# Performance work log

Measured on AMD Instinct MI355X. Metric: run time of the kernel, lower is better.

## Reference

```python
import jax, jax.numpy as jnp
import numpy as np

K = 100
TEMPERATURE = 1.0


def setup_inputs() -> dict:
    key = jax.random.key(0)
    k1, k2, k3 = jax.random.split(key, 3)
    student_emb = jax.random.normal(k1, (8, 512, 1500), dtype=jnp.float32)
    teacher_codes = jax.random.randint(k2, (8, 1500), 0, 4096, dtype=jnp.int64)
    codebook = jax.random.normal(k3, (4096, 512), dtype=jnp.float32)
    return {"student_emb": student_emb, "teacher_codes": teacher_codes, "codebook": codebook}


def reference(student_emb, teacher_codes, codebook):
    B, C, T = student_emb.shape
    # flatten tokens: (N, C) with N = B*T
    emb = jnp.transpose(student_emb, (0, 2, 1)).reshape(-1, C)
    codes = teacher_codes.reshape(-1).astype(jnp.int32)

    # Euclidean cdist via the ||a||^2 + ||b||^2 - 2ab expansion (same math as torch.cdist)
    emb_sq = jnp.sum(emb * emb, axis=1, keepdims=True)            # (N,1)
    cb_sq = jnp.sum(codebook * codebook, axis=1)[None, :]         # (1,V)
    d2 = emb_sq + cb_sq - 2.0 * jnp.matmul(emb, codebook.T)       # (N,V)
    distances = jnp.sqrt(jnp.maximum(d2, 0.0))

    # top-k smallest distances
    _, top_k_indices = jax.lax.top_k(-distances, K)               # (N,K)

    # include_correct: replace last candidate with the true code if absent
    correct_in_topk = jnp.any(top_k_indices == codes[:, None], axis=1)
    top_k_indices = top_k_indices.at[:, -1].set(
        jnp.where(correct_in_topk, top_k_indices[:, -1], codes))

    candidate_distances = jnp.take_along_axis(distances, top_k_indices, axis=1)
    logits = -candidate_distances / TEMPERATURE                   # (N,K)

    match = top_k_indices == codes[:, None]
    local_labels = jnp.argmax(match.astype(jnp.int32), axis=1)    # (N,)

    logp = jax.nn.log_softmax(logits, axis=1)
    loss = -jnp.mean(jnp.take_along_axis(logp, local_labels[:, None], axis=1))

    local_predictions = jnp.argmax(logits, axis=-1)
    local_accuracy = jnp.mean((local_predictions == local_labels).astype(jnp.float32))
    global_predictions = jnp.argmin(distances, axis=-1)
    global_accuracy = jnp.mean((global_predictions == codes).astype(jnp.float32))
    correct_in_candidates = jnp.mean(jnp.any(top_k_indices == codes[:, None], axis=1).astype(jnp.float32))

    return loss, local_accuracy, global_accuracy, correct_in_candidates
```

## Files before the change

### kernel.cpp

```cpp
#include <hip/hip_runtime.h>
#include <hip/hip_bf16.h>
#include <cstdint>

#define B_ 8
#define C_ 512
#define T_ 1500
#define N_ (B_*T_)
#define NPAD_ 12032
#define V_ 4096
#define K_ 100

typedef unsigned long long u64;
typedef __attribute__((ext_vector_type(8))) short short8;
typedef __attribute__((ext_vector_type(8))) unsigned short u16x8;
typedef __attribute__((ext_vector_type(4))) float f32x4;

__device__ __forceinline__ unsigned short f2bf(float x){
    __hip_bfloat16 h = __float2bfloat16(x);
    return __builtin_bit_cast(unsigned short, h);
}
__device__ __forceinline__ unsigned short f2h(float x){
    return __builtin_bit_cast(unsigned short, (_Float16)x);
}
__device__ __forceinline__ float h2f(unsigned short h){
    return (float)__builtin_bit_cast(_Float16, h);
}

__device__ __forceinline__ void gll16(const unsigned short* g, unsigned short* l){
    __builtin_amdgcn_global_load_lds(
        (const __attribute__((address_space(1))) void*)g,
        (__attribute__((address_space(3))) void*)l, 16, 0, 0);
}

__global__ __launch_bounds__(256) void cbconv_kernel(const float* __restrict__ CB,
                                                     unsigned short* __restrict__ CBh,
                                                     float* __restrict__ csq){
    int wv = threadIdx.x >> 6, lane = threadIdx.x & 63;
    int r = blockIdx.x * 4 + wv;
    const float4* p4 = (const float4*)(CB + (size_t)r * C_);
    ushort4* o4 = (ushort4*)(CBh + (size_t)r * C_);
    float s = 0.f;
    #pragma unroll
    for (int j = 0; j < 2; ++j){
        float4 v = p4[lane + j*64];
        s += v.x*v.x + v.y*v.y + v.z*v.z + v.w*v.w;
        ushort4 h; h.x = f2bf(v.x); h.y = f2bf(v.y); h.z = f2bf(v.z); h.w = f2bf(v.w);
        o4[lane + j*64] = h;
    }
    #pragma unroll
    for (int o = 32; o; o >>= 1) s += __shfl_down(s, o, 64);
    if (lane == 0) csq[r] = s;
}

__global__ __launch_bounds__(256) void transpose_conv_kernel(const float* __restrict__ S,
                                                             unsigned short* __restrict__ embT,
                                                             float* __restrict__ esq){
    __shared__ float tile[32][33];
    __shared__ float psum[8][33];
    int b  = blockIdx.z;
    int c0 = blockIdx.y * 32;
    int t0 = blockIdx.x * 32;
    int tx = threadIdx.x, ty = threadIdx.y;
    #pragma unroll
    for (int r = 0; r < 4; ++r){
        int c = c0 + ty + r*8;
        int t = t0 + tx;
        tile[ty + r*8][tx] = (t < T_) ? S[((size_t)b*C_ + c)*T_ + t] : 0.f;
    }
    __syncthreads();
    float ps = 0.f;
    #pragma unroll
    for (int r = 0; r < 4; ++r){ float v = tile[ty + r*8][tx]; ps += v * v; }
    psum[ty][tx] = ps;
    #pragma unroll
    for (int r = 0; r < 4; ++r){
        int t = t0 + ty + r*8;
        int c = c0 + tx;
        if (t < T_) embT[((size_t)b*T_ + t)*C_ + c] = f2bf(tile[tx][ty + r*8]);
    }
    __syncthreads();
    if (ty == 0){
        int t = t0 + tx;
        if (t < T_){
            float s2 = 0.f;
            #pragma unroll
            for (int w = 0; w < 8; ++w) s2 += psum[w][tx];
            atomicAdd(&esq[b*T_ + t], s2);
        }
    }
}

__global__ __launch_bounds__(256) void gemm_dot_kernel(
    const unsigned short* __restrict__ A, const unsigned short* __restrict__ Bm,
    unsigned short* __restrict__ doth, int row_lo, int row_hi)
{
    __shared__ unsigned short smem[128*136];
    unsigned short* As = smem;
    unsigned short* Bs = smem + 128*32;
    int tid = threadIdx.x, lane = tid & 63, wv = tid >> 6;
    int row0 = row_lo + blockIdx.x * 128;
    int col0 = blockIdx.y * 128;

    int sr = lane >> 2;
    int sk = (lane & 3) * 8;
    int ar0 = row0 + wv*32 + sr;       int ar1 = ar0 + 16;
    int ca0 = (ar0 < N_) ? ar0 : N_-1; int ca1 = (ar1 < N_) ? ar1 : N_-1;
    const unsigned short* Ap0 = A  + (size_t)ca0 * C_ + sk;
    const unsigned short* Ap1 = A  + (size_t)ca1 * C_ + sk;
    const unsigned short* Bp0 = Bm + (size_t)(col0 + wv*32 + sr) * C_ + sk;
    const unsigned short* Bp1 = Bp0 + (size_t)16 * C_;
    unsigned short* Ad0 = &As[(wv*32     ) * 32];
    unsigned short* Ad1 = &As[(wv*32 + 16) * 32];
    unsigned short* Bd0 = &Bs[(wv*32     ) * 32];
    unsigned short* Bd1 = &Bs[(wv*32 + 16) * 32];

    int wm = (wv >> 1) * 64, wn = (wv & 1) * 64;
    int fr = lane & 15;
    int fk = (lane >> 4) * 8;

    f32x4 acc[4][4];
    #pragma unroll
    for (int i = 0; i < 4; ++i)
        #pragma unroll
        for (int j = 0; j < 4; ++j) acc[i][j] = (f32x4){0.f, 0.f, 0.f, 0.f};

    for (int kt = 0; kt < C_/32; ++kt){
        int k0 = kt * 32;
        gll16(Ap0 + k0, Ad0);
        gll16(Ap1 + k0, Ad1);
        gll16(Bp0 + k0, Bd0);
        gll16(Bp1 + k0, Bd1);
        __syncthreads();
        short8 af[4], bf[4];
        #pragma unroll
        for (int i = 0; i < 4; ++i) af[i] = *(const short8*)&As[(wm + i*16 + fr)*32 + fk];
        #pragma unroll
        for (int j = 0; j < 4; ++j) bf[j] = *(const short8*)&Bs[(wn + j*16 + fr)*32 + fk];
        #pragma unroll
        for (int i = 0; i < 4; ++i)
            #pragma unroll
            for (int j = 0; j < 4; ++j)
                acc[i][j] = __builtin_amdgcn_mfma_f32_16x16x32_bf16(bf[j], af[i], acc[i][j], 0, 0, 0);
        __syncthreads();
    }

    const int LD = 136;
    int en = lane & 15;
    int ev = (lane >> 4) * 4;
    #pragma unroll
    for (int i = 0; i < 4; ++i){
        int r = wm + i*16 + en;
        #pragma unroll
        for (int j = 0; j < 4; ++j){
            ushort4 h;
            h.x = f2h(acc[i][j][0]);
            h.y = f2h(acc[i][j][1]);
            h.z = f2h(acc[i][j][2]);
            h.w = f2h(acc[i][j][3]);
            *(ushort4*)&smem[r*LD + wn + j*16 + ev] = h;
        }
    }
    __syncthreads();

    int rr = tid >> 4;
    int cc = (tid & 15) * 8;
    #pragma unroll
    for (int it = 0; it < 8; ++it){
        int r = it*16 + rr;
        int n = row0 + r;
        if (n < row_hi){
            u16x8 v = *(const u16x8*)&smem[r*LD + cc];
            *(u16x8*)&doth[(size_t)(n - row_lo) * V_ + col0 + cc] = v;
        }
    }
}

__global__ __launch_bounds__(256, 2) void select_kernel(const unsigned short* __restrict__ doth,
                                                        const int* __restrict__ codes,
                                                        const float* __restrict__ esq,
                                                        const float* __restrict__ csq,
                                                        float2* __restrict__ pairbuf,
                                                        int row_lo, int nrows){
    int tid = threadIdx.x, lane = tid & 63, wv = tid >> 6;
    int lrow = blockIdx.x * 4 + wv;
    if (lrow >= nrows) return;
    int n = row_lo + lrow;
    const u16x8* r8 = (const u16x8*)(doth + (size_t)lrow * V_);

    __shared__ unsigned hist[4][256] __attribute__((aligned(16)));
    __shared__ unsigned coll[4][64];
    __shared__ unsigned collcnt[4];

    float esq_n = esq[n];
    int code = codes[n];
    float dotc = h2f(doth[(size_t)lrow * V_ + code]);
    unsigned ucode = __float_as_uint(fmaxf(esq_n + csq[code] - 2.f * dotc, 0.f));

    unsigned u[64];
    #pragma unroll
    for (int j = 0; j < 8; ++j){
        u16x8 h = r8[lane + j*64];
        const float4* cp = (const float4*)(csq + 8*lane + 512*j);
        float4 c0 = cp[0], c1 = cp[1];
        float cs[8] = {c0.x, c0.y, c0.z, c0.w, c1.x, c1.y, c1.z, c1.w};
        #pragma unroll
        for (int e = 0; e < 8; ++e){
            float d2 = fmaxf(esq_n + cs[e] - 2.f * h2f(h[e]), 0.f);
            u[8*j+e] = __float_as_uint(d2);
        }
    }

    unsigned umin = u[0], umax = u[0];
    #pragma unroll
    for (int k = 1; k < 64; ++k){
        umin = (u[k] < umin) ? u[k] : umin;
        umax = (u[k] > umax) ? u[k] : umax;
    }
    #pragma unroll
    for (int o = 32; o; o >>= 1){
        unsigned a = (unsigned)__shfl_xor((int)umin, o, 64); if (a < umin) umin = a;
        unsigned b = (unsigned)__shfl_xor((int)umax, o, 64); if (b > umax) umax = b;
    }
    unsigned im = 0xFFFFFFFFu;
    #pragma unroll
    for (int k = 0; k < 64; ++k){
        unsigned idx = 8u*(unsigned)lane + (unsigned)(512*(k >> 3) + (k & 7));
        if (u[k] == umin && idx < im) im = idx;
    }
    #pragma unroll
    for (int o = 32; o; o >>= 1){
        unsigned a = (unsigned)__shfl_xor((int)im, o, 64); if (a < im) im = a;
    }
    int idx0 = (int)im;
    float d0 = sqrtf(__uint_as_float(umin));

    unsigned t;
    if (umin == umax){
        t = umin;
    } else {
        ((uint4*)&hist[wv][0])[lane] = (uint4){0u,0u,0u,0u};
        if (lane == 0) collcnt[wv] = 0u;
        asm volatile("s_waitcnt lgkmcnt(0)" ::: "memory");
        float fmn = __uint_as_float(umin), fmx = __uint_as_float(umax);
        float invw = 256.0f / (fmx - fmn);
        #pragma unroll
        for (int k = 0; k < 64; ++k){
            float fk = __uint_as_float(u[k]);
            int b = (int)((fk - fmn) * invw); b = (b > 255) ? 255 : b;
            atomicAdd(&hist[wv][b], 1u);
        }
        asm volatile("s_waitcnt lgkmcnt(0)" ::: "memory");
        uint4 hq = ((uint4*)&hist[wv][0])[lane];
        unsigned lsum = hq.x + hq.y + hq.z + hq.w;
        unsigned inc = lsum;
        #pragma unroll
        for (int o = 1; o < 64; o <<= 1){
            unsigned y = (unsigned)__shfl_up((int)inc, o, 64);
            if (lane >= o) inc += y;
        }
        unsigned e0 = inc - lsum;
        unsigned e1 = e0 + hq.x, e2 = e1 + hq.y, e3 = e2 + hq.z, e4 = e3 + hq.w;
        int sel = -1;
        if      (e0 <= 99u && 99u < e1) sel = 0;
        else if (e1 <= 99u && 99u < e2) sel = 1;
        else if (e2 <= 99u && 99u < e3) sel = 2;
        else if (e3 <= 99u && 99u < e4) sel = 3;
        u64 bal = __ballot(sel >= 0);
        int src = __ffsll(bal) - 1;
        unsigned myBk = (unsigned)(4*lane + (sel < 0 ? 0 : sel));
        unsigned myBase = (sel == 1) ? e1 : (sel == 2) ? e2 : (sel == 3) ? e3 : e0;
        int Bk   = __shfl((int)myBk,   src, 64);
        int base = __shfl((int)myBase, src, 64);
        int rk = 99 - base;
        #pragma unroll
        for (int k = 0; k < 64; ++k){
            float fk = __uint_as_float(u[k]);
            int b = (int)((fk - fmn) * invw); b = (b > 255) ? 255 : b;
            if (b == Bk){
                unsigned pos = atomicAdd(&collcnt[wv], 1u);
                if (pos < 64u) coll[wv][pos] = u[k];
            }
        }
        asm volatile("s_waitcnt lgkmcnt(0)" ::: "memory");
        unsigned bcnt = collcnt[wv];
        if (bcnt <= 64u){
            unsigned w = (lane < (int)bcnt) ? coll[wv][lane] : 0xFFFFFFFFu;
            unsigned wmn = (lane < (int)bcnt) ? w : 0xFFFFFFFFu;
            unsigned wmx = (lane < (int)bcnt) ? w : 0u;
            #pragma unroll
            for (int o = 32; o; o >>= 1){
                unsigned a = (unsigned)__shfl_xor((int)wmn, o, 64); if (a < wmn) wmn = a;
                unsigned b = (unsigned)__shfl_xor((int)wmx, o, 64); if (b > wmx) wmx = b;
            }
            unsigned P;
            if (wmn == wmx) P = wmn;
            else {
                int hb = 31 - __clz((int)(wmn ^ wmx));
                unsigned mask = (hb == 31) ? 0xFFFFFFFFu : ((1u << (hb+1)) - 1u);
                P = wmn & ~mask;
                for (int b = hb; b >= 0; --b){
                    unsigned cand = P | (1u << b);
                    int c = __popcll(__ballot(w < cand));
                    if (c <= rk) P = cand;
                }
            }
            t = P;
        } else {
            int hb = 31 - __clz((int)(umin ^ umax));
            unsigned mask = (hb == 31) ? 0xFFFFFFFFu : ((1u << (hb+1)) - 1u);
            unsigned P = umin & ~mask;
            for (int b = hb; b >= 0; --b){
                unsigned cand = P | (1u << b);
                int c = 0;
                #pragma unroll
                for (int k = 0; k < 64; ++k) c += (u[k] < cand) ? 1 : 0;
                #pragma unroll
                for (int o = 32; o; o >>= 1) c += __shfl_xor(c, o, 64);
                if (c <= 99) P = cand;
            }
            t = P;
        }
    }
    float tval = sqrtf(__uint_as_float(t));

    float s = 0.f; int cl = 0;
    #pragma unroll
    for (int k = 0; k < 64; ++k){
        if (u[k] < t){ s += __expf(d0 - sqrtf(__uint_as_float(u[k]))); cl++; }
    }
    #pragma unroll
    for (int o = 32; o; o >>= 1){
        s += __shfl_xor(s, o, 64);
        cl += __shfl_xor(cl, o, 64);
    }
    if (lane == 0){
        float S = s + (float)(K_ - cl) * __expf(d0 - tval);
        float dcode = sqrtf(__uint_as_float(ucode));
        if (ucode > t) S += __expf(d0 - dcode) - __expf(d0 - tval);
        float nll = dcode - d0 + __logf(S);
        pairbuf[n] = make_float2(nll, (idx0 == code) ? 1.f : 0.f);
    }
}

__global__ __launch_bounds__(1024) void finalize_kernel(const float2* __restrict__ pair,
                                                        float* __restrict__ out){
    int tid = threadIdx.x;
    float sn = 0.f, sh = 0.f;
    for (int i = tid; i < N_; i += 1024){
        float2 p = pair[i]; sn += p.x; sh += p.y;
    }
    #pragma unroll
    for (int o = 32; o; o >>= 1){ sn += __shfl_down(sn, o, 64); sh += __shfl_down(sh, o, 64); }
    __shared__ float a[16], b[16];
    int wv = tid >> 6, lane = tid & 63;
    if (lane == 0){ a[wv] = sn; b[wv] = sh; }
    __syncthreads();
    if (tid == 0){
        float L = 0.f, H = 0.f;
        #pragma unroll
        for (int i = 0; i < 16; ++i){ L += a[i]; H += b[i]; }
        out[0] = L / (float)N_;
        out[1] = H / (float)N_;
        out[2] = H / (float)N_;
        out[3] = 1.0f;
    }
}

extern "C" void kernel_launch(void* const* d_in, const int* in_sizes, int n_in,
                              void* d_out, int out_size, void* d_ws, size_t ws_size,
                              hipStream_t stream){
    const float* S   = (const float*)d_in[0];
    const int* codes = (const int*)d_in[1];
    const float* CB  = (const float*)d_in[2];
    float* out = (float*)d_out;

    char* w = (char*)d_ws;
    size_t off = 0;
    unsigned short* embT = (unsigned short*)(w + off); off += (size_t)NPAD_ * C_ * 2;
    unsigned short* CBh  = (unsigned short*)(w + off); off += (size_t)V_ * C_ * 2;
    float* csq = (float*)(w + off); off += (size_t)V_ * 4;
    float* esq = (float*)(w + off); off += (size_t)N_ * 4;
    off = (off + 255) & ~(size_t)255;
    float2* pairbuf = (float2*)(w + off); off += (size_t)N_ * 8;
    unsigned short* dotbuf = (unsigned short*)(w + off);

    size_t avail = (ws_size > off) ? ws_size - off : 0;
    long maxrows = (long)(avail / ((size_t)V_ * 2));

    hipMemsetAsync(esq, 0, (size_t)N_ * 4, stream);
    hipLaunchKernelGGL(cbconv_kernel, dim3(V_/4), dim3(256), 0, stream, CB, CBh, csq);
    hipLaunchKernelGGL(transpose_conv_kernel, dim3((T_+31)/32, C_/32, B_), dim3(32, 8), 0, stream,
                       S, embT, esq);

    if (maxrows >= N_){
        const int gchunk = 3072;
        for (int row_lo = 0; row_lo < N_; row_lo += gchunk){
            int row_hi = row_lo + gchunk; if (row_hi > N_) row_hi = N_;
            int rows = row_hi - row_lo;
            hipLaunchKernelGGL(gemm_dot_kernel, dim3((rows + 127)/128, V_/128), dim3(256), 0, stream,
                               embT, CBh, dotbuf + (size_t)row_lo * V_, row_lo, row_hi);
        }
        hipLaunchKernelGGL(select_kernel, dim3((N_ + 3)/4), dim3(256), 0, stream,
                           dotbuf, codes, esq, csq, pairbuf, 0, N_);
    } else {
        int chunk = (int)(maxrows & ~127L);
        if (chunk < 128) chunk = 128;
        for (int row_lo = 0; row_lo < N_; row_lo += chunk){
            int row_hi = row_lo + chunk; if (row_hi > N_) row_hi = N_;
            int rows = row_hi - row_lo;
            hipLaunchKernelGGL(gemm_dot_kernel, dim3((rows + 127)/128, V_/128), dim3(256), 0, stream,
                               embT, CBh, dotbuf, row_lo, row_hi);
            hipLaunchKernelGGL(select_kernel, dim3((rows + 3)/4), dim3(256), 0, stream,
                               dotbuf, codes, esq, csq, pairbuf, row_lo, rows);
        }
    }
    hipLaunchKernelGGL(finalize_kernel, dim3(1), dim3(1024), 0, stream, pairbuf, out);
}
```

Before: 225.3 us.

## Fuse argmin into min/max reduction and compute softmax sum from compacted candidates

The select kernel now tracks the argmin index during the min/max pass and reduces value and index together. This removes a second 64-element scan and its shuffle reduction. Histogram bins are packed into registers so they are not recomputed. While collecting the threshold bin, the kernel also collects elements from lower bins into a second LDS list, so the softmax partial sum needs only a few exp/sqrt per lane instead of a predicated sweep over all 64 values; the old sweep is kept as a fallback. The GEMM launch chunk is doubled, which means fewer launches; the extra LDS and atomics could cost some occupancy.

```diff
diff --git a/kernel.cpp b/kernel.cpp
--- a/kernel.cpp
+++ b/kernel.cpp
@@ -189,7 +189,8 @@
 
     __shared__ unsigned hist[4][256] __attribute__((aligned(16)));
     __shared__ unsigned coll[4][64];
-    __shared__ unsigned collcnt[4];
+    __shared__ unsigned coll2[4][128];
+    __shared__ unsigned cnts[4][2];
 
     float esq_n = esq[n];
     int code = codes[n];
@@ -210,43 +211,47 @@
         }
     }
 
-    unsigned umin = u[0], umax = u[0];
+    unsigned vmin = u[0], vmax = u[0];
+    int kmin = 0;
     #pragma unroll
     for (int k = 1; k < 64; ++k){
-        umin = (u[k] < umin) ? u[k] : umin;
-        umax = (u[k] > umax) ? u[k] : umax;
-    }
+        if (u[k] < vmin){ vmin = u[k]; kmin = k; }
+        vmax = (u[k] > vmax) ? u[k] : vmax;
+    }
+    unsigned im = 8u*(unsigned)lane + (unsigned)(512*(kmin >> 3) + (kmin & 7));
     #pragma unroll
     for (int o = 32; o; o >>= 1){
-        unsigned a = (unsigned)__shfl_xor((int)umin, o, 64); if (a < umin) umin = a;
-        unsigned b = (unsigned)__shfl_xor((int)umax, o, 64); if (b > umax) umax = b;
-    }
-    unsigned im = 0xFFFFFFFFu;
-    #pragma unroll
-    for (int k = 0; k < 64; ++k){
-        unsigned idx = 8u*(unsigned)lane + (unsigned)(512*(k >> 3) + (k & 7));
-        if (u[k] == umin && idx < im) im = idx;
-    }
-    #pragma unroll
-    for (int o = 32; o; o >>= 1){
-        unsigned a = (unsigned)__shfl_xor((int)im, o, 64); if (a < im) im = a;
-    }
+        unsigned v2 = (unsigned)__shfl_xor((int)vmin, o, 64);
+        unsigned i2 = (unsigned)__shfl_xor((int)im,   o, 64);
+        if (v2 < vmin || (v2 == vmin && i2 < im)){ vmin = v2; im = i2; }
+        unsigned b2 = (unsigned)__shfl_xor((int)vmax, o, 64);
+        if (b2 > vmax) vmax = b2;
+    }
+    unsigned umin = vmin, umax = vmax;
     int idx0 = (int)im;
     float d0 = sqrtf(__uint_as_float(umin));
 
     unsigned t;
+    int base = 0, bcnt = 0;
+    unsigned w = 0xFFFFFFFFu;
+    bool fb = false;
     if (umin == umax){
         t = umin;
     } else {
         ((uint4*)&hist[wv][0])[lane] = (uint4){0u,0u,0u,0u};
-        if (lane == 0) collcnt[wv] = 0u;
+        if (lane < 2) cnts[wv][lane] = 0u;
         asm volatile("s_waitcnt lgkmcnt(0)" ::: "memory");
         float fmn = __uint_as_float(umin), fmx = __uint_as_float(umax);
         float invw = 256.0f / (fmx - fmn);
+        float nb = -fmn * invw;
+        unsigned bp[16];
+        #pragma unroll
+        for (int r = 0; r < 16; ++r) bp[r] = 0u;
         #pragma unroll
         for (int k = 0; k < 64; ++k){
-            float fk = __uint_as_float(u[k]);
-            int b = (int)((fk - fmn) * invw); b = (b > 255) ? 255 : b;
+            int b = (int)fmaf(__uint_as_float(u[k]), invw, nb);
+            b = (b > 255) ? 255 : b;
+            bp[k >> 2] |= (unsigned)b << ((k & 3) * 8);
             atomicAdd(&hist[wv][b], 1u);
         }
         asm volatile("s_waitcnt lgkmcnt(0)" ::: "memory");
@@ -269,28 +274,30 @@
         int src = __ffsll(bal) - 1;
         unsigned myBk = (unsigned)(4*lane + (sel < 0 ? 0 : sel));
         unsigned myBase = (sel == 1) ? e1 : (sel == 2) ? e2 : (sel == 3) ? e3 : e0;
-        int Bk   = __shfl((int)myBk,   src, 64);
-        int base = __shfl((int)myBase, src, 64);
+        int Bk = __shfl((int)myBk,   src, 64);
+        base   = __shfl((int)myBase, src, 64);
         int rk = 99 - base;
         #pragma unroll
         for (int k = 0; k < 64; ++k){
-            float fk = __uint_as_float(u[k]);
-            int b = (int)((fk - fmn) * invw); b = (b > 255) ? 255 : b;
+            int b = (int)((bp[k >> 2] >> ((k & 3) * 8)) & 255u);
             if (b == Bk){
-                unsigned pos = atomicAdd(&collcnt[wv], 1u);
+                unsigned pos = atomicAdd(&cnts[wv][0], 1u);
                 if (pos < 64u) coll[wv][pos] = u[k];
+            } else if (b < Bk){
+                unsigned pos = atomicAdd(&cnts[wv][1], 1u);
+                if (pos < 128u) coll2[wv][pos] = u[k];
             }
         }
         asm volatile("s_waitcnt lgkmcnt(0)" ::: "memory");
-        unsigned bcnt = collcnt[wv];
-        if (bcnt <= 64u){
-            unsigned w = (lane < (int)bcnt) ? coll[wv][lane] : 0xFFFFFFFFu;
-            unsigned wmn = (lane < (int)bcnt) ? w : 0xFFFFFFFFu;
-            unsigned wmx = (lane < (int)bcnt) ? w : 0u;
+        bcnt = (int)cnts[wv][0];
+        if (bcnt <= 64){
+            w = (lane < bcnt) ? coll[wv][lane] : 0xFFFFFFFFu;
+            unsigned wmn = (lane < bcnt) ? w : 0xFFFFFFFFu;
+            unsigned wmx = (lane < bcnt) ? w : 0u;
             #pragma unroll
             for (int o = 32; o; o >>= 1){
                 unsigned a = (unsigned)__shfl_xor((int)wmn, o, 64); if (a < wmn) wmn = a;
-                unsigned b = (unsigned)__shfl_xor((int)wmx, o, 64); if (b > wmx) wmx = b;
+                unsigned b2 = (unsigned)__shfl_xor((int)wmx, o, 64); if (b2 > wmx) wmx = b2;
             }
             unsigned P;
             if (wmn == wmx) P = wmn;
@@ -298,19 +305,20 @@
                 int hb = 31 - __clz((int)(wmn ^ wmx));
                 unsigned mask = (hb == 31) ? 0xFFFFFFFFu : ((1u << (hb+1)) - 1u);
                 P = wmn & ~mask;
-                for (int b = hb; b >= 0; --b){
-                    unsigned cand = P | (1u << b);
+                for (int b2 = hb; b2 >= 0; --b2){
+                    unsigned cand = P | (1u << b2);
                     int c = __popcll(__ballot(w < cand));
                     if (c <= rk) P = cand;
                 }
             }
             t = P;
         } else {
+            fb = true;
             int hb = 31 - __clz((int)(umin ^ umax));
             unsigned mask = (hb == 31) ? 0xFFFFFFFFu : ((1u << (hb+1)) - 1u);
             unsigned P = umin & ~mask;
-            for (int b = hb; b >= 0; --b){
-                unsigned cand = P | (1u << b);
+            for (int b2 = hb; b2 >= 0; --b2){
+                unsigned cand = P | (1u << b2);
                 int c = 0;
                 #pragma unroll
                 for (int k = 0; k < 64; ++k) c += (u[k] < cand) ? 1 : 0;
@@ -324,15 +332,32 @@
     float tval = sqrtf(__uint_as_float(t));
 
     float s = 0.f; int cl = 0;
-    #pragma unroll
-    for (int k = 0; k < 64; ++k){
-        if (u[k] < t){ s += __expf(d0 - sqrtf(__uint_as_float(u[k]))); cl++; }
-    }
-    #pragma unroll
-    for (int o = 32; o; o >>= 1){
-        s += __shfl_xor(s, o, 64);
-        cl += __shfl_xor(cl, o, 64);
-    }
+    if (fb){
+        #pragma unroll
+        for (int k = 0; k < 64; ++k){
+            if (u[k] < t){ s += __expf(d0 - sqrtf(__uint_as_float(u[k]))); cl++; }
+        }
+        #pragma unroll
+        for (int o = 32; o; o >>= 1){
+            s += __shfl_xor(s, o, 64);
+            cl += __shfl_xor(cl, o, 64);
+        }
+    } else {
+        int c_in = (int)__popcll(__ballot(w < t));
+        cl = base + c_in;
+        #pragma unroll
+        for (int r = 0; r < 2; ++r){
+            int ix = lane + 64*r;
+            if (ix < base){
+                float vv = __uint_as_float(coll2[wv][ix]);
+                s += __expf(d0 - sqrtf(vv));
+            }
+        }
+        if (w < t) s += __expf(d0 - sqrtf(__uint_as_float(w)));
+        #pragma unroll
+        for (int o = 32; o; o >>= 1) s += __shfl_xor(s, o, 64);
+    }
+
     if (lane == 0){
         float S = s + (float)(K_ - cl) * __expf(d0 - tval);
         float dcode = sqrtf(__uint_as_float(ucode));
@@ -393,7 +418,7 @@
                        S, embT, esq);
 
     if (maxrows >= N_){
-        const int gchunk = 3072;
+        const int gchunk = 6144;
         for (int row_lo = 0; row_lo < N_; row_lo += gchunk){
             int row_hi = row_lo + gchunk; if (row_hi > N_) row_hi = N_;
             int rows = row_hi - row_lo;
```

After: 213.9 us. -5.0%, faster.
